# Kernel optimization log

Measured on AMD Instinct MI355X. Metric: run time of the kernel, lower is better.

The kernel has to match this reference:

```python
import jax, jax.numpy as jnp
import numpy as np

EMB = 1024
HEADS = 16
HD = EMB // HEADS

def setup_inputs() -> dict:
    key = jax.random.key(0)
    ks = jax.random.split(key, 9)
    s = 1.0 / np.sqrt(EMB)
    x = jax.random.normal(ks[0], (4, 2048, EMB), dtype=jnp.float32)
    Wq = jax.random.uniform(ks[1], (EMB, EMB), jnp.float32, -s, s)
    bq = jax.random.uniform(ks[2], (EMB,), jnp.float32, -s, s)
    Wk = jax.random.uniform(ks[3], (EMB, EMB), jnp.float32, -s, s)
    bk = jax.random.uniform(ks[4], (EMB,), jnp.float32, -s, s)
    Wv = jax.random.uniform(ks[5], (EMB, EMB), jnp.float32, -s, s)
    bv = jax.random.uniform(ks[6], (EMB,), jnp.float32, -s, s)
    Wo = jax.random.uniform(ks[7], (EMB, EMB), jnp.float32, -s, s)
    bo = jax.random.uniform(ks[8], (EMB,), jnp.float32, -s, s)
    return {"x": x, "Wq": Wq, "bq": bq, "Wk": Wk, "bk": bk, "Wv": Wv, "bv": bv, "Wo": Wo, "bo": bo}

def reference(x, Wq, bq, Wk, bk, Wv, bv, Wo, bo):
    B, T, C = x.shape
    # projections (torch Linear: y = x @ W^T + b)
    q = (x @ Wq.T + bq).reshape(B, T, HEADS, HD).transpose(0, 2, 1, 3)  # [B,H,T,hd]
    k = (x @ Wk.T + bk).reshape(B, T, HEADS, HD).transpose(0, 2, 1, 3)
    v = (x @ Wv.T + bv).reshape(B, T, HEADS, HD).transpose(0, 2, 1, 3)
    scores = jnp.einsum('bhqd,bhkd->bhqk', q, k) / jnp.sqrt(jnp.float32(HD))
    weights = jax.nn.softmax(scores, axis=-1)
    attn = jnp.einsum('bhqk,bhkd->bhqd', weights, v)
    out = attn.transpose(0, 2, 1, 3).reshape(B, T, C)
    return out @ Wo.T + bo
```

## Files before the change

kernel.cpp:

```cpp
#include <hip/hip_runtime.h>

#define TSEQ  2048
#define BATCH 4
#define NHEAD 16
#define EMB   1024

typedef __attribute__((ext_vector_type(8))) __bf16 bf16x8;
typedef __attribute__((ext_vector_type(4))) __bf16 bf16x4;
typedef __attribute__((ext_vector_type(4))) float  floatx4;
typedef __attribute__((ext_vector_type(2))) unsigned int uint32x2;
typedef __attribute__((ext_vector_type(4))) unsigned int uint32x4;

__device__ __forceinline__ void gload_lds16(const __bf16* g, __bf16* lds_uniform_base) {
  __builtin_amdgcn_global_load_lds(
      (__attribute__((address_space(1))) void*)(g),
      (__attribute__((address_space(3))) void*)(lds_uniform_base),
      16, 0, 0);
}

__global__ __launch_bounds__(256) void cvt_f32_bf16(
    const float* __restrict__ src, __bf16* __restrict__ dst)
{
  const int gid = (blockIdx.x * 256 + threadIdx.x) * 4;
  const float4 v = *(const float4*)(src + gid);
  dst[gid + 0] = (__bf16)v.x;
  dst[gid + 1] = (__bf16)v.y;
  dst[gid + 2] = (__bf16)v.z;
  dst[gid + 3] = (__bf16)v.w;
}

__global__ __launch_bounds__(256) void cvt_w4(
    const float* __restrict__ s0, const float* __restrict__ s1,
    const float* __restrict__ s2, const float* __restrict__ s3,
    __bf16* __restrict__ d0, __bf16* __restrict__ d1,
    __bf16* __restrict__ d2, __bf16* __restrict__ d3)
{
  const int z = blockIdx.z;
  const float* src = (z == 0) ? s0 : (z == 1) ? s1 : (z == 2) ? s2 : s3;
  __bf16*      dst = (z == 0) ? d0 : (z == 1) ? d1 : (z == 2) ? d2 : d3;
  const int gid = (blockIdx.x * 256 + threadIdx.x) * 4;
  const float4 v = *(const float4*)(src + gid);
  dst[gid + 0] = (__bf16)v.x;
  dst[gid + 1] = (__bf16)v.y;
  dst[gid + 2] = (__bf16)v.z;
  dst[gid + 3] = (__bf16)v.w;
}

__global__ __launch_bounds__(256) void gemm_bt_bias(
    const __bf16* __restrict__ A,
    const __bf16* __restrict__ W0, const __bf16* __restrict__ W1, const __bf16* __restrict__ W2,
    const float* __restrict__ B0, const float* __restrict__ B1, const float* __restrict__ B2,
    __bf16* __restrict__ C0, __bf16* __restrict__ C1, __bf16* __restrict__ C2)
{
  const int z = blockIdx.z;
  const __bf16* W  = (z == 0) ? W0 : ((z == 1) ? W1 : W2);
  const float*  Bb = (z == 0) ? B0 : ((z == 1) ? B1 : B2);
  __bf16*       C  = (z == 0) ? C0 : ((z == 1) ? C1 : C2);
  const float  scl = (z == 0) ? 0.125f * 1.44269504088896340736f : 1.0f;

  const int tid  = threadIdx.x;
  const int lane = tid & 63;
  const int wid  = tid >> 6;
  const int l16  = lane & 15;
  const int quad = lane >> 4;
  const int wm   = wid & 1;
  const int wn   = wid >> 1;
  const int lin = blockIdx.x + blockIdx.y * 8;
  const int swz = (lin & 7) * 64 + (lin >> 3);
  const int m0  = (swz >> 3) * 128;
  const int n0  = (swz & 7) * 128;

  __shared__ alignas(16) __bf16 As[128 * 32];
  __shared__ alignas(16) __bf16 Bs[128 * 32];

  floatx4 acc[4][4];
#pragma unroll
  for (int i = 0; i < 4; i++)
#pragma unroll
    for (int j = 0; j < 4; j++) acc[i][j] = (floatx4){0.f, 0.f, 0.f, 0.f};

  const int srow = tid >> 2;
  const int sseg = tid & 3;

  for (int k0 = 0; k0 < 1024; k0 += 32) {
    __syncthreads();
#pragma unroll
    for (int is = 0; is < 2; is++) {
      const int row = is * 64 + srow;
      gload_lds16(A + (size_t)(m0 + row) * 1024 + k0 + sseg * 8,
                  &As[(is * 256 + wid * 64) * 8]);
      gload_lds16(W + (size_t)(n0 + row) * 1024 + k0 + sseg * 8,
                  &Bs[(is * 256 + wid * 64) * 8]);
    }
    __syncthreads();

    bf16x8 af[4], bfr[4];
#pragma unroll
    for (int i = 0; i < 4; i++) {
      af[i]  = *(const bf16x8*)(&As[(wm * 64 + i * 16 + l16) * 32 + quad * 8]);
      bfr[i] = *(const bf16x8*)(&Bs[(wn * 64 + i * 16 + l16) * 32 + quad * 8]);
    }
#pragma unroll
    for (int i = 0; i < 4; i++)
#pragma unroll
      for (int j = 0; j < 4; j++)
        acc[i][j] = __builtin_amdgcn_mfma_f32_16x16x32_bf16(af[i], bfr[j], acc[i][j], 0, 0, 0);
  }

  float bv[4];
#pragma unroll
  for (int j = 0; j < 4; j++) bv[j] = Bb[n0 + wn * 64 + j * 16 + l16];

#pragma unroll
  for (int i = 0; i < 4; i++) {
    const size_t mrow = (size_t)m0 + wm * 64 + i * 16 + quad * 4;
#pragma unroll
    for (int j = 0; j < 4; j++) {
      const int col = n0 + wn * 64 + j * 16 + l16;
#pragma unroll
      for (int r = 0; r < 4; r++)
        C[(mrow + r) * 1024 + col] = (__bf16)((acc[i][j][r] + bv[j]) * scl);
    }
  }
}

__global__ __launch_bounds__(256) void gemm_bt_bias_f32(
    const __bf16* __restrict__ A, const __bf16* __restrict__ W,
    const float* __restrict__ Bb, float* __restrict__ C)
{
  const int tid  = threadIdx.x;
  const int lane = tid & 63;
  const int wid  = tid >> 6;
  const int l16  = lane & 15;
  const int quad = lane >> 4;
  const int wm   = wid & 1;
  const int wn   = wid >> 1;
  const int lin = blockIdx.x + blockIdx.y * 8;
  const int swz = (lin & 7) * 64 + (lin >> 3);
  const int m0  = (swz >> 3) * 128;
  const int n0  = (swz & 7) * 128;

  __shared__ alignas(16) __bf16 As[128 * 32];
  __shared__ alignas(16) __bf16 Bs[128 * 32];

  floatx4 acc[4][4];
#pragma unroll
  for (int i = 0; i < 4; i++)
#pragma unroll
    for (int j = 0; j < 4; j++) acc[i][j] = (floatx4){0.f, 0.f, 0.f, 0.f};

  const int srow = tid >> 2;
  const int sseg = tid & 3;

  for (int k0 = 0; k0 < 1024; k0 += 32) {
    __syncthreads();
#pragma unroll
    for (int is = 0; is < 2; is++) {
      const int row = is * 64 + srow;
      gload_lds16(A + (size_t)(m0 + row) * 1024 + k0 + sseg * 8,
                  &As[(is * 256 + wid * 64) * 8]);
      gload_lds16(W + (size_t)(n0 + row) * 1024 + k0 + sseg * 8,
                  &Bs[(is * 256 + wid * 64) * 8]);
    }
    __syncthreads();

    bf16x8 af[4], bfr[4];
#pragma unroll
    for (int i = 0; i < 4; i++) {
      af[i]  = *(const bf16x8*)(&As[(wm * 64 + i * 16 + l16) * 32 + quad * 8]);
      bfr[i] = *(const bf16x8*)(&Bs[(wn * 64 + i * 16 + l16) * 32 + quad * 8]);
    }
#pragma unroll
    for (int i = 0; i < 4; i++)
#pragma unroll
      for (int j = 0; j < 4; j++)
        acc[i][j] = __builtin_amdgcn_mfma_f32_16x16x32_bf16(af[i], bfr[j], acc[i][j], 0, 0, 0);
  }

  float bv[4];
#pragma unroll
  for (int j = 0; j < 4; j++) bv[j] = Bb[n0 + wn * 64 + j * 16 + l16];

#pragma unroll
  for (int i = 0; i < 4; i++) {
    const size_t mrow = (size_t)m0 + wm * 64 + i * 16 + quad * 4;
#pragma unroll
    for (int j = 0; j < 4; j++) {
      const int col = n0 + wn * 64 + j * 16 + l16;
#pragma unroll
      for (int r = 0; r < 4; r++)
        C[(mrow + r) * 1024 + col] = acc[i][j][r] + bv[j];
    }
  }
}

__global__ __launch_bounds__(256) void v_transpose(
    const __bf16* __restrict__ V, __bf16* __restrict__ VT)
{
  const int t0 = blockIdx.x * 64;
  const int bh = blockIdx.y;
  const int b  = bh >> 4;
  const int h  = bh & 15;
  const int tid = threadIdx.x;

  __shared__ alignas(16) __bf16 Ls[64 * 72];

  const int row = tid >> 2, seg = tid & 3;
  const __bf16* src = V + ((size_t)(b * TSEQ + t0 + row)) * EMB + h * 64;
  *(bf16x8*)(&Ls[row * 72 + seg * 8])       = *(const bf16x8*)(src + seg * 8);
  *(bf16x8*)(&Ls[row * 72 + (seg + 4) * 8]) = *(const bf16x8*)(src + (seg + 4) * 8);
  __syncthreads();

  const int od = tid >> 2, oseg = tid & 3;
  bf16x8 o0, o1;
#pragma unroll
  for (int j = 0; j < 8; j++) o0[j] = Ls[(oseg * 16 + j) * 72 + od];
#pragma unroll
  for (int j = 0; j < 8; j++) o1[j] = Ls[(oseg * 16 + 8 + j) * 72 + od];
  __bf16* dst = VT + ((size_t)bh * 64 + od) * TSEQ + t0 + oseg * 16;
  *(bf16x8*)(dst)     = o0;
  *(bf16x8*)(dst + 8) = o1;
}

#define KVB 64
#define NT  (TSEQ / KVB)

#define FA_ZERO (floatx4){0.f, 0.f, 0.f, 0.f}

#define FA_STAGE(BUF, TILE)                                                               \
  if ((TILE) < NT) {                                                                      \
    _Pragma("unroll")                                                                     \
    for (int c = 0; c < 2; c++) {                                                         \
      gload_lds16(kstage + (size_t)((TILE) * KVB + c * 8) * EMB,                          \
                  &Ks[BUF][(wid * 16 + c * 8) * 64]);                                     \
      gload_lds16(vstage + (size_t)(c * 8) * TSEQ + (TILE) * KVB,                         \
                  &VTs[BUF][(wid * 16 + c * 8) * 64]);                                    \
    }                                                                                     \
  }

#define SM_PACK(TA, TB, DST)                                                              \
  {                                                                                       \
    bf16x4 pa_, pb_;                                                                      \
    _Pragma("unroll")                                                                     \
    for (int r = 0; r < 4; r++) pa_[r] = (__bf16)__builtin_amdgcn_exp2f((TA)[r]);         \
    _Pragma("unroll")                                                                     \
    for (int r = 0; r < 4; r++) pb_[r] = (__bf16)__builtin_amdgcn_exp2f((TB)[r]);         \
    const uint32x2 A2_ = __builtin_bit_cast(uint32x2, pa_);                               \
    const uint32x2 B2_ = __builtin_bit_cast(uint32x2, pb_);                               \
    const uint32x2 r0_ = __builtin_amdgcn_permlane32_swap(A2_.x, B2_.x, false, false);    \
    const uint32x2 r1_ = __builtin_amdgcn_permlane32_swap(A2_.y, B2_.y, false, false);    \
    const uint32x2 s0_ = __builtin_amdgcn_permlane16_swap(r0_.x, r0_.y, false, false);    \
    const uint32x2 s1_ = __builtin_amdgcn_permlane16_swap(r1_.x, r1_.y, false, false);    \
    const uint32x4 fw_ = (uint32x4){s0_.x, s1_.x, s0_.y, s1_.y};                          \
    DST = __builtin_bit_cast(bf16x8, fw_);                                                \
  }

#define QK_BLOCK(BUF, KS, TA, TB)                                                         \
  {                                                                                       \
    const bf16x8 ka0 = *(const bf16x8*)(&Ks[BUF][(KS) * 2048 + aoff0]);                   \
    const bf16x8 ka1 = *(const bf16x8*)(&Ks[BUF][(KS) * 2048 + aoff1]);                   \
    const bf16x8 kb0 = *(const bf16x8*)(&Ks[BUF][(KS) * 2048 + 1024 + aoff0]);            \
    const bf16x8 kb1 = *(const bf16x8*)(&Ks[BUF][(KS) * 2048 + 1024 + aoff1]);            \
    _Pragma("unroll")                                                                     \
    for (int g = 0; g < 4; g++) {                                                         \
      TA[g] = FA_ZERO;                                                                    \
      TA[g] = __builtin_amdgcn_mfma_f32_16x16x32_bf16(ka0, qf[g][0], TA[g], 0, 0, 0);     \
      TA[g] = __builtin_amdgcn_mfma_f32_16x16x32_bf16(ka1, qf[g][1], TA[g], 0, 0, 0);     \
      TB[g] = FA_ZERO;                                                                    \
      TB[g] = __builtin_amdgcn_mfma_f32_16x16x32_bf16(kb0, qf[g][0], TB[g], 0, 0, 0);     \
      TB[g] = __builtin_amdgcn_mfma_f32_16x16x32_bf16(kb1, qf[g][1], TB[g], 0, 0, 0);     \
    }                                                                                     \
  }

#define FA_STEP(BUF, KT)                                                                  \
  {                                                                                       \
    __builtin_amdgcn_s_setprio(1);                                                        \
    bf16x8 vf[4][2];                                                                      \
    _Pragma("unroll")                                                                     \
    for (int dg = 0; dg < 4; dg++) {                                                      \
      vf[dg][0] = *(const bf16x8*)(&VTs[(BUF) ^ 1][dg * 1024 + aoff0]);                   \
      vf[dg][1] = *(const bf16x8*)(&VTs[(BUF) ^ 1][dg * 1024 + aoff1]);                   \
    }                                                                                     \
    floatx4 ta[4], tb[4];                                                                 \
    QK_BLOCK(BUF, 0, ta, tb)                                                              \
    _Pragma("unroll")                                                                     \
    for (int g = 0; g < 4; g++) {                                                         \
      bf16x8 nf;                                                                          \
      SM_PACK(ta[g], tb[g], nf)                                                           \
      _Pragma("unroll")                                                                   \
      for (int dg = 0; dg < 4; dg++)                                                      \
        Oacc[g][dg] = __builtin_amdgcn_mfma_f32_16x16x32_bf16(vf[dg][0], pfragP[g][0], Oacc[g][dg], 0, 0, 0); \
      lacc[g] = __builtin_amdgcn_mfma_f32_16x16x32_bf16(ones, pfragP[g][0], lacc[g], 0, 0, 0); \
      _Pragma("unroll")                                                                   \
      for (int dg = 0; dg < 4; dg++)                                                      \
        Oacc[g][dg] = __builtin_amdgcn_mfma_f32_16x16x32_bf16(vf[dg][1], pfragP[g][1], Oacc[g][dg], 0, 0, 0); \
      lacc[g] = __builtin_amdgcn_mfma_f32_16x16x32_bf16(ones, pfragP[g][1], lacc[g], 0, 0, 0); \
      pfragP[g][0] = nf;                                                                  \
    }                                                                                     \
    QK_BLOCK(BUF, 1, ta, tb)                                                              \
    __builtin_amdgcn_s_setprio(0);                                                        \
    __syncthreads();                                                                      \
    FA_STAGE((BUF) ^ 1, (KT) + 1);                                                        \
    _Pragma("unroll")                                                                     \
    for (int g = 0; g < 4; g++) { SM_PACK(ta[g], tb[g], pfragP[g][1]) }                   \
    __syncthreads();                                                                      \
  }

__global__ __launch_bounds__(256, 2) void flash_attn(
    const __bf16* __restrict__ Q, const __bf16* __restrict__ K,
    const __bf16* __restrict__ VT, __bf16* __restrict__ O)
{
  const int lin = blockIdx.x + blockIdx.y * 8;
  const int swz = (lin & 7) * 64 + (lin >> 3);
  const int qt  = swz & 7;
  const int bh  = swz >> 3;
  const int b    = bh >> 4;
  const int h    = bh & 15;
  const int tid  = threadIdx.x;
  const int wid  = tid >> 6;
  const int lane = tid & 63;
  const int l16  = lane & 15;
  const int quad = lane >> 4;

  __shared__ alignas(16) __bf16 Ks[2][KVB * 64];
  __shared__ alignas(16) __bf16 VTs[2][64 * 64];

  const size_t base = ((size_t)b * TSEQ) * EMB + (size_t)h * 64;
  const __bf16* qptr  = Q + base;
  const __bf16* kptr  = K + base;
  const __bf16* vtptr = VT + (size_t)bh * 64 * TSEQ;
  __bf16*       optr  = O + base;

  const int qb = qt * 256 + wid * 64;

  bf16x8 qf[4][2];
#pragma unroll
  for (int g = 0; g < 4; g++)
#pragma unroll
    for (int hf = 0; hf < 2; hf++)
      qf[g][hf] = *(const bf16x8*)(qptr + (size_t)(qb + g * 16 + l16) * EMB + hf * 32 + quad * 8);

  floatx4 Oacc[4][4];
#pragma unroll
  for (int g = 0; g < 4; g++)
#pragma unroll
    for (int dg = 0; dg < 4; dg++) Oacc[g][dg] = FA_ZERO;
  floatx4 lacc[4];
#pragma unroll
  for (int g = 0; g < 4; g++) lacc[g] = FA_ZERO;

  const uint32x4 onesw = (uint32x4){0x3F803F80u, 0x3F803F80u, 0x3F803F80u, 0x3F803F80u};
  const bf16x8 ones = __builtin_bit_cast(bf16x8, onesw);

  const int lrow = lane >> 3;
  const int xsg  = (lane & 7) ^ lrow;
  const __bf16* kstage = kptr  + (size_t)(wid * 16 + lrow) * EMB  + xsg * 8;
  const __bf16* vstage = vtptr + (size_t)(wid * 16 + lrow) * TSEQ + xsg * 8;

  const int h7    = l16 & 7;
  const int x0    = quad ^ h7;
  const int aoff0 = l16 * 64 + x0 * 8;
  const int aoff1 = l16 * 64 + (x0 ^ 4) * 8;

  bf16x8 pfragP[4][2];

  FA_STAGE(0, 0);
  __syncthreads();
  FA_STAGE(1, 1);
  {
    floatx4 ta[4], tb[4];
    QK_BLOCK(0, 0, ta, tb)
#pragma unroll
    for (int g = 0; g < 4; g++) { SM_PACK(ta[g], tb[g], pfragP[g][0]) }
    QK_BLOCK(0, 1, ta, tb)
#pragma unroll
    for (int g = 0; g < 4; g++) { SM_PACK(ta[g], tb[g], pfragP[g][1]) }
  }
  __syncthreads();

#pragma unroll 1
  for (int kt = 1; kt < NT - 1; kt += 2) {
    FA_STEP(1, kt);
    FA_STEP(0, kt + 1);
  }
  FA_STEP(1, NT - 1);

#pragma unroll
  for (int g = 0; g < 4; g++) {
#pragma unroll
    for (int dg = 0; dg < 4; dg++) {
      const bf16x8 v0 = *(const bf16x8*)(&VTs[1][dg * 1024 + aoff0]);
      const bf16x8 v1 = *(const bf16x8*)(&VTs[1][dg * 1024 + aoff1]);
      Oacc[g][dg] = __builtin_amdgcn_mfma_f32_16x16x32_bf16(v0, pfragP[g][0], Oacc[g][dg], 0, 0, 0);
      Oacc[g][dg] = __builtin_amdgcn_mfma_f32_16x16x32_bf16(v1, pfragP[g][1], Oacc[g][dg], 0, 0, 0);
    }
    lacc[g] = __builtin_amdgcn_mfma_f32_16x16x32_bf16(ones, pfragP[g][0], lacc[g], 0, 0, 0);
    lacc[g] = __builtin_amdgcn_mfma_f32_16x16x32_bf16(ones, pfragP[g][1], lacc[g], 0, 0, 0);
  }

#pragma unroll
  for (int g = 0; g < 4; g++) {
    const float inv = 1.0f / lacc[g][0];
#pragma unroll
    for (int dg = 0; dg < 4; dg++) {
      bf16x4 ov;
#pragma unroll
      for (int r = 0; r < 4; r++) ov[r] = (__bf16)(Oacc[g][dg][r] * inv);
      *(bf16x4*)(optr + (size_t)(qb + g * 16 + l16) * EMB + dg * 16 + quad * 4) = ov;
    }
  }
}

extern "C" void kernel_launch(void* const* d_in, const int* in_sizes, int n_in,
                              void* d_out, int out_size, void* d_ws, size_t ws_size,
                              hipStream_t stream) {
  const float* x  = (const float*)d_in[0];
  const float* Wq = (const float*)d_in[1];
  const float* bq = (const float*)d_in[2];
  const float* Wk = (const float*)d_in[3];
  const float* bk = (const float*)d_in[4];
  const float* Wv = (const float*)d_in[5];
  const float* bv = (const float*)d_in[6];
  const float* Wo = (const float*)d_in[7];
  const float* bo = (const float*)d_in[8];
  float* out = (float*)d_out;

  const size_t NELEM = (size_t)BATCH * TSEQ * EMB;
  const size_t WELEM = (size_t)EMB * EMB;

  __bf16* q_b  = (__bf16*)d_out;
  __bf16* k_b  = q_b + NELEM;
  __bf16* x_b  = (__bf16*)d_ws;
  __bf16* v_b  = x_b + NELEM;
  __bf16* wq_b = v_b + NELEM;
  __bf16* wk_b = wq_b + WELEM;
  __bf16* wv_b = wk_b + WELEM;
  __bf16* wo_b = wv_b + WELEM;

  dim3 blk(256, 1, 1);

  cvt_f32_bf16<<<(int)(NELEM / 1024), blk, 0, stream>>>(x, x_b);
  cvt_w4<<<dim3((int)(WELEM / 1024), 1, 4), blk, 0, stream>>>(
      Wq, Wk, Wv, Wo, wq_b, wk_b, wv_b, wo_b);

  gemm_bt_bias<<<dim3(8, 64, 3), blk, 0, stream>>>(
      x_b, wq_b, wk_b, wv_b, bq, bk, bv, q_b, k_b, v_b);

  v_transpose<<<dim3(TSEQ / 64, BATCH * NHEAD), blk, 0, stream>>>(v_b, x_b);

  flash_attn<<<dim3(TSEQ / 256, BATCH * NHEAD), blk, 0, stream>>>(
      q_b, k_b, x_b, v_b);

  gemm_bt_bias_f32<<<dim3(8, 64, 1), blk, 0, stream>>>(v_b, wo_b, bo, out);
}
```

Measured before the change: 261.1 us.

## Double-buffer GEMM with swizzled LDS and shrink flash-attention query tile

The QKV and output GEMMs now share a macro body that uses a 64-wide K tile, double-buffered LDS with XOR-swizzled rows, and explicit vmcnt waits, so global loads overlap MFMA work and LDS bank conflicts drop. Flash attention is cut from 256 to 128 query rows per block, 32 per wave, which doubles the grid and lowers register pressure. V fragments are also read from LDS inside the MFMA loop instead of being preloaded. The trade-offs are more LDS per GEMM block, twice the K/V tile reloads in attention, and correctness that depends on the hand-written waitcnt and barrier sequence.

```diff
diff --git a/kernel.cpp b/kernel.cpp
--- a/kernel.cpp
+++ b/kernel.cpp
@@ -46,6 +46,89 @@
   dst[gid + 3] = (__bf16)v.w;
 }
 
+#define GK_NT 16
+
+#define GEMM_STAGE(BUF, K0)                                                               \
+  {                                                                                       \
+    _Pragma("unroll")                                                                     \
+    for (int c = 0; c < 4; c++) {                                                         \
+      gload_lds16(aStage + (size_t)(c * 32) * 1024 + (K0),                                \
+                  &As[BUF][(c * 32 + wid * 8) * 64]);                                     \
+      gload_lds16(bStage + (size_t)(c * 32) * 1024 + (K0),                                \
+                  &Bs[BUF][(c * 32 + wid * 8) * 64]);                                     \
+    }                                                                                     \
+  }
+
+#define GEMM_BODY(C_STORE)                                                                \
+  const int tid  = threadIdx.x;                                                           \
+  const int lane = tid & 63;                                                              \
+  const int wid  = tid >> 6;                                                              \
+  const int l16  = lane & 15;                                                             \
+  const int quad = lane >> 4;                                                             \
+  const int wm   = wid & 1;                                                               \
+  const int wn   = wid >> 1;                                                              \
+  const int lin = blockIdx.x + blockIdx.y * 8;                                            \
+  const int swz = (lin & 7) * 64 + (lin >> 3);                                            \
+  const int m0  = (swz >> 3) * 128;                                                       \
+  const int n0  = (swz & 7) * 128;                                                        \
+  __shared__ alignas(16) __bf16 As[2][128 * 64];                                          \
+  __shared__ alignas(16) __bf16 Bs[2][128 * 64];                                          \
+  floatx4 acc[4][4];                                                                      \
+  _Pragma("unroll")                                                                       \
+  for (int i = 0; i < 4; i++)                                                             \
+    _Pragma("unroll")                                                                     \
+    for (int j = 0; j < 4; j++) acc[i][j] = (floatx4){0.f, 0.f, 0.f, 0.f};                \
+  const int lrow = lane >> 3;                                                             \
+  const int xsg  = (lane & 7) ^ lrow;                                                     \
+  const __bf16* aStage = A + (size_t)(m0 + wid * 8 + lrow) * 1024 + xsg * 8;              \
+  const __bf16* bStage = W + (size_t)(n0 + wid * 8 + lrow) * 1024 + xsg * 8;              \
+  const int h7 = l16 & 7;                                                                 \
+  GEMM_STAGE(0, 0)                                                                        \
+  GEMM_STAGE(1, 64)                                                                       \
+  __asm__ __volatile__("s_waitcnt vmcnt(8)\n\ts_barrier" ::: "memory");                   \
+  int cur = 0;                                                                            \
+  _Pragma("unroll 1")                                                                     \
+  for (int k = 0; k < GK_NT; ++k) {                                                       \
+    bf16x8 af0[4], af1[4], bf0[4], bf1[4];                                                \
+    _Pragma("unroll")                                                                     \
+    for (int i = 0; i < 4; i++) {                                                         \
+      const int ar = (wm * 64 + i * 16 + l16) * 64;                                       \
+      const int br = (wn * 64 + i * 16 + l16) * 64;                                       \
+      af0[i] = *(const bf16x8*)(&As[cur][ar + ((quad ^ h7)) * 8]);                        \
+      af1[i] = *(const bf16x8*)(&As[cur][ar + (((4 + quad) ^ h7)) * 8]);                  \
+      bf0[i] = *(const bf16x8*)(&Bs[cur][br + ((quad ^ h7)) * 8]);                        \
+      bf1[i] = *(const bf16x8*)(&Bs[cur][br + (((4 + quad) ^ h7)) * 8]);                  \
+    }                                                                                     \
+    _Pragma("unroll")                                                                     \
+    for (int i = 0; i < 4; i++)                                                           \
+      _Pragma("unroll")                                                                   \
+      for (int j = 0; j < 4; j++) {                                                       \
+        acc[i][j] = __builtin_amdgcn_mfma_f32_16x16x32_bf16(af0[i], bf0[j], acc[i][j], 0, 0, 0); \
+        acc[i][j] = __builtin_amdgcn_mfma_f32_16x16x32_bf16(af1[i], bf1[j], acc[i][j], 0, 0, 0); \
+      }                                                                                   \
+    __asm__ __volatile__("s_waitcnt lgkmcnt(0)\n\ts_barrier" ::: "memory");               \
+    if (k < GK_NT - 2) {                                                                  \
+      GEMM_STAGE(cur, (k + 2) * 64)                                                       \
+      __asm__ __volatile__("s_waitcnt vmcnt(8)\n\ts_barrier" ::: "memory");               \
+    } else if (k == GK_NT - 2) {                                                          \
+      __asm__ __volatile__("s_waitcnt vmcnt(0)\n\ts_barrier" ::: "memory");               \
+    }                                                                                     \
+    cur ^= 1;                                                                             \
+  }                                                                                       \
+  float bv[4];                                                                            \
+  _Pragma("unroll")                                                                       \
+  for (int j = 0; j < 4; j++) bv[j] = Bb[n0 + wn * 64 + j * 16 + l16];                    \
+  _Pragma("unroll")                                                                       \
+  for (int i = 0; i < 4; i++) {                                                           \
+    const size_t mrow = (size_t)m0 + wm * 64 + i * 16 + quad * 4;                         \
+    _Pragma("unroll")                                                                     \
+    for (int j = 0; j < 4; j++) {                                                         \
+      const int col = n0 + wn * 64 + j * 16 + l16;                                        \
+      _Pragma("unroll")                                                                   \
+      for (int r = 0; r < 4; r++) C_STORE;                                                \
+    }                                                                                     \
+  }
+
 __global__ __launch_bounds__(256) void gemm_bt_bias(
     const __bf16* __restrict__ A,
     const __bf16* __restrict__ W0, const __bf16* __restrict__ W1, const __bf16* __restrict__ W2,
@@ -57,141 +140,14 @@
   const float*  Bb = (z == 0) ? B0 : ((z == 1) ? B1 : B2);
   __bf16*       C  = (z == 0) ? C0 : ((z == 1) ? C1 : C2);
   const float  scl = (z == 0) ? 0.125f * 1.44269504088896340736f : 1.0f;
-
-  const int tid  = threadIdx.x;
-  const int lane = tid & 63;
-  const int wid  = tid >> 6;
-  const int l16  = lane & 15;
-  const int quad = lane >> 4;
-  const int wm   = wid & 1;
-  const int wn   = wid >> 1;
-  const int lin = blockIdx.x + blockIdx.y * 8;
-  const int swz = (lin & 7) * 64 + (lin >> 3);
-  const int m0  = (swz >> 3) * 128;
-  const int n0  = (swz & 7) * 128;
-
-  __shared__ alignas(16) __bf16 As[128 * 32];
-  __shared__ alignas(16) __bf16 Bs[128 * 32];
-
-  floatx4 acc[4][4];
-#pragma unroll
-  for (int i = 0; i < 4; i++)
-#pragma unroll
-    for (int j = 0; j < 4; j++) acc[i][j] = (floatx4){0.f, 0.f, 0.f, 0.f};
-
-  const int srow = tid >> 2;
-  const int sseg = tid & 3;
-
-  for (int k0 = 0; k0 < 1024; k0 += 32) {
-    __syncthreads();
-#pragma unroll
-    for (int is = 0; is < 2; is++) {
-      const int row = is * 64 + srow;
-      gload_lds16(A + (size_t)(m0 + row) * 1024 + k0 + sseg * 8,
-                  &As[(is * 256 + wid * 64) * 8]);
-      gload_lds16(W + (size_t)(n0 + row) * 1024 + k0 + sseg * 8,
-                  &Bs[(is * 256 + wid * 64) * 8]);
-    }
-    __syncthreads();
-
-    bf16x8 af[4], bfr[4];
-#pragma unroll
-    for (int i = 0; i < 4; i++) {
-      af[i]  = *(const bf16x8*)(&As[(wm * 64 + i * 16 + l16) * 32 + quad * 8]);
-      bfr[i] = *(const bf16x8*)(&Bs[(wn * 64 + i * 16 + l16) * 32 + quad * 8]);
-    }
-#pragma unroll
-    for (int i = 0; i < 4; i++)
-#pragma unroll
-      for (int j = 0; j < 4; j++)
-        acc[i][j] = __builtin_amdgcn_mfma_f32_16x16x32_bf16(af[i], bfr[j], acc[i][j], 0, 0, 0);
-  }
-
-  float bv[4];
-#pragma unroll
-  for (int j = 0; j < 4; j++) bv[j] = Bb[n0 + wn * 64 + j * 16 + l16];
-
-#pragma unroll
-  for (int i = 0; i < 4; i++) {
-    const size_t mrow = (size_t)m0 + wm * 64 + i * 16 + quad * 4;
-#pragma unroll
-    for (int j = 0; j < 4; j++) {
-      const int col = n0 + wn * 64 + j * 16 + l16;
-#pragma unroll
-      for (int r = 0; r < 4; r++)
-        C[(mrow + r) * 1024 + col] = (__bf16)((acc[i][j][r] + bv[j]) * scl);
-    }
-  }
+  GEMM_BODY(C[(mrow + r) * 1024 + col] = (__bf16)((acc[i][j][r] + bv[j]) * scl))
 }
 
 __global__ __launch_bounds__(256) void gemm_bt_bias_f32(
     const __bf16* __restrict__ A, const __bf16* __restrict__ W,
     const float* __restrict__ Bb, float* __restrict__ C)
 {
-  const int tid  = threadIdx.x;
-  const int lane = tid & 63;
-  const int wid  = tid >> 6;
-  const int l16  = lane & 15;
-  const int quad = lane >> 4;
-  const int wm   = wid & 1;
-  const int wn   = wid >> 1;
-  const int lin = blockIdx.x + blockIdx.y * 8;
-  const int swz = (lin & 7) * 64 + (lin >> 3);
-  const int m0  = (swz >> 3) * 128;
-  const int n0  = (swz & 7) * 128;
-
-  __shared__ alignas(16) __bf16 As[128 * 32];
-  __shared__ alignas(16) __bf16 Bs[128 * 32];
-
-  floatx4 acc[4][4];
-#pragma unroll
-  for (int i = 0; i < 4; i++)
-#pragma unroll
-    for (int j = 0; j < 4; j++) acc[i][j] = (floatx4){0.f, 0.f, 0.f, 0.f};
-
-  const int srow = tid >> 2;
-  const int sseg = tid & 3;
-
-  for (int k0 = 0; k0 < 1024; k0 += 32) {
-    __syncthreads();
-#pragma unroll
-    for (int is = 0; is < 2; is++) {
-      const int row = is * 64 + srow;
-      gload_lds16(A + (size_t)(m0 + row) * 1024 + k0 + sseg * 8,
-                  &As[(is * 256 + wid * 64) * 8]);
-      gload_lds16(W + (size_t)(n0 + row) * 1024 + k0 + sseg * 8,
-                  &Bs[(is * 256 + wid * 64) * 8]);
-    }
-    __syncthreads();
-
-    bf16x8 af[4], bfr[4];
-#pragma unroll
-    for (int i = 0; i < 4; i++) {
-      af[i]  = *(const bf16x8*)(&As[(wm * 64 + i * 16 + l16) * 32 + quad * 8]);
-      bfr[i] = *(const bf16x8*)(&Bs[(wn * 64 + i * 16 + l16) * 32 + quad * 8]);
-    }
-#pragma unroll
-    for (int i = 0; i < 4; i++)
-#pragma unroll
-      for (int j = 0; j < 4; j++)
-        acc[i][j] = __builtin_amdgcn_mfma_f32_16x16x32_bf16(af[i], bfr[j], acc[i][j], 0, 0, 0);
-  }
-
-  float bv[4];
-#pragma unroll
-  for (int j = 0; j < 4; j++) bv[j] = Bb[n0 + wn * 64 + j * 16 + l16];
-
-#pragma unroll
-  for (int i = 0; i < 4; i++) {
-    const size_t mrow = (size_t)m0 + wm * 64 + i * 16 + quad * 4;
-#pragma unroll
-    for (int j = 0; j < 4; j++) {
-      const int col = n0 + wn * 64 + j * 16 + l16;
-#pragma unroll
-      for (int r = 0; r < 4; r++)
-        C[(mrow + r) * 1024 + col] = acc[i][j][r] + bv[j];
-    }
-  }
+  GEMM_BODY(C[(mrow + r) * 1024 + col] = acc[i][j][r] + bv[j])
 }
 
 __global__ __launch_bounds__(256) void v_transpose(
@@ -262,7 +218,7 @@
     const bf16x8 kb0 = *(const bf16x8*)(&Ks[BUF][(KS) * 2048 + 1024 + aoff0]);            \
     const bf16x8 kb1 = *(const bf16x8*)(&Ks[BUF][(KS) * 2048 + 1024 + aoff1]);            \
     _Pragma("unroll")                                                                     \
-    for (int g = 0; g < 4; g++) {                                                         \
+    for (int g = 0; g < 2; g++) {                                                         \
       TA[g] = FA_ZERO;                                                                    \
       TA[g] = __builtin_amdgcn_mfma_f32_16x16x32_bf16(ka0, qf[g][0], TA[g], 0, 0, 0);     \
       TA[g] = __builtin_amdgcn_mfma_f32_16x16x32_bf16(ka1, qf[g][1], TA[g], 0, 0, 0);     \
@@ -275,25 +231,23 @@
 #define FA_STEP(BUF, KT)                                                                  \
   {                                                                                       \
     __builtin_amdgcn_s_setprio(1);                                                        \
-    bf16x8 vf[4][2];                                                                      \
-    _Pragma("unroll")                                                                     \
-    for (int dg = 0; dg < 4; dg++) {                                                      \
-      vf[dg][0] = *(const bf16x8*)(&VTs[(BUF) ^ 1][dg * 1024 + aoff0]);                   \
-      vf[dg][1] = *(const bf16x8*)(&VTs[(BUF) ^ 1][dg * 1024 + aoff1]);                   \
-    }                                                                                     \
-    floatx4 ta[4], tb[4];                                                                 \
+    floatx4 ta[2], tb[2];                                                                 \
     QK_BLOCK(BUF, 0, ta, tb)                                                              \
     _Pragma("unroll")                                                                     \
-    for (int g = 0; g < 4; g++) {                                                         \
+    for (int g = 0; g < 2; g++) {                                                         \
       bf16x8 nf;                                                                          \
       SM_PACK(ta[g], tb[g], nf)                                                           \
       _Pragma("unroll")                                                                   \
-      for (int dg = 0; dg < 4; dg++)                                                      \
-        Oacc[g][dg] = __builtin_amdgcn_mfma_f32_16x16x32_bf16(vf[dg][0], pfragP[g][0], Oacc[g][dg], 0, 0, 0); \
+      for (int dg = 0; dg < 4; dg++) {                                                    \
+        const bf16x8 v0 = *(const bf16x8*)(&VTs[(BUF) ^ 1][dg * 1024 + aoff0]);           \
+        Oacc[g][dg] = __builtin_amdgcn_mfma_f32_16x16x32_bf16(v0, pfragP[g][0], Oacc[g][dg], 0, 0, 0); \
+      }                                                                                   \
       lacc[g] = __builtin_amdgcn_mfma_f32_16x16x32_bf16(ones, pfragP[g][0], lacc[g], 0, 0, 0); \
       _Pragma("unroll")                                                                   \
-      for (int dg = 0; dg < 4; dg++)                                                      \
-        Oacc[g][dg] = __builtin_amdgcn_mfma_f32_16x16x32_bf16(vf[dg][1], pfragP[g][1], Oacc[g][dg], 0, 0, 0); \
+      for (int dg = 0; dg < 4; dg++) {                                                    \
+        const bf16x8 v1 = *(const bf16x8*)(&VTs[(BUF) ^ 1][dg * 1024 + aoff1]);           \
+        Oacc[g][dg] = __builtin_amdgcn_mfma_f32_16x16x32_bf16(v1, pfragP[g][1], Oacc[g][dg], 0, 0, 0); \
+      }                                                                                   \
       lacc[g] = __builtin_amdgcn_mfma_f32_16x16x32_bf16(ones, pfragP[g][1], lacc[g], 0, 0, 0); \
       pfragP[g][0] = nf;                                                                  \
     }                                                                                     \
@@ -302,7 +256,7 @@
     __syncthreads();                                                                      \
     FA_STAGE((BUF) ^ 1, (KT) + 1);                                                        \
     _Pragma("unroll")                                                                     \
-    for (int g = 0; g < 4; g++) { SM_PACK(ta[g], tb[g], pfragP[g][1]) }                   \
+    for (int g = 0; g < 2; g++) { SM_PACK(ta[g], tb[g], pfragP[g][1]) }                   \
     __syncthreads();                                                                      \
   }
 
@@ -310,10 +264,10 @@
     const __bf16* __restrict__ Q, const __bf16* __restrict__ K,
     const __bf16* __restrict__ VT, __bf16* __restrict__ O)
 {
-  const int lin = blockIdx.x + blockIdx.y * 8;
-  const int swz = (lin & 7) * 64 + (lin >> 3);
-  const int qt  = swz & 7;
-  const int bh  = swz >> 3;
+  const int lin = blockIdx.x + blockIdx.y * 16;
+  const int swz = (lin & 7) * 128 + (lin >> 3);
+  const int qt  = swz & 15;
+  const int bh  = swz >> 4;
   const int b    = bh >> 4;
   const int h    = bh & 15;
   const int tid  = threadIdx.x;
@@ -331,23 +285,23 @@
   const __bf16* vtptr = VT + (size_t)bh * 64 * TSEQ;
   __bf16*       optr  = O + base;
 
-  const int qb = qt * 256 + wid * 64;
-
-  bf16x8 qf[4][2];
-#pragma unroll
-  for (int g = 0; g < 4; g++)
+  const int qb = qt * 128 + wid * 32;
+
+  bf16x8 qf[2][2];
+#pragma unroll
+  for (int g = 0; g < 2; g++)
 #pragma unroll
     for (int hf = 0; hf < 2; hf++)
       qf[g][hf] = *(const bf16x8*)(qptr + (size_t)(qb + g * 16 + l16) * EMB + hf * 32 + quad * 8);
 
-  floatx4 Oacc[4][4];
-#pragma unroll
-  for (int g = 0; g < 4; g++)
+  floatx4 Oacc[2][4];
+#pragma unroll
+  for (int g = 0; g < 2; g++)
 #pragma unroll
     for (int dg = 0; dg < 4; dg++) Oacc[g][dg] = FA_ZERO;
-  floatx4 lacc[4];
-#pragma unroll
-  for (int g = 0; g < 4; g++) lacc[g] = FA_ZERO;
+  floatx4 lacc[2];
+#pragma unroll
+  for (int g = 0; g < 2; g++) lacc[g] = FA_ZERO;
 
   const uint32x4 onesw = (uint32x4){0x3F803F80u, 0x3F803F80u, 0x3F803F80u, 0x3F803F80u};
   const bf16x8 ones = __builtin_bit_cast(bf16x8, onesw);
@@ -362,19 +316,19 @@
   const int aoff0 = l16 * 64 + x0 * 8;
   const int aoff1 = l16 * 64 + (x0 ^ 4) * 8;
 
-  bf16x8 pfragP[4][2];
+  bf16x8 pfragP[2][2];
 
   FA_STAGE(0, 0);
   __syncthreads();
   FA_STAGE(1, 1);
   {
-    floatx4 ta[4], tb[4];
+    floatx4 ta[2], tb[2];
     QK_BLOCK(0, 0, ta, tb)
 #pragma unroll
-    for (int g = 0; g < 4; g++) { SM_PACK(ta[g], tb[g], pfragP[g][0]) }
+    for (int g = 0; g < 2; g++) { SM_PACK(ta[g], tb[g], pfragP[g][0]) }
     QK_BLOCK(0, 1, ta, tb)
 #pragma unroll
-    for (int g = 0; g < 4; g++) { SM_PACK(ta[g], tb[g], pfragP[g][1]) }
+    for (int g = 0; g < 2; g++) { SM_PACK(ta[g], tb[g], pfragP[g][1]) }
   }
   __syncthreads();
 
@@ -386,7 +340,7 @@
   FA_STEP(1, NT - 1);
 
 #pragma unroll
-  for (int g = 0; g < 4; g++) {
+  for (int g = 0; g < 2; g++) {
 #pragma unroll
     for (int dg = 0; dg < 4; dg++) {
       const bf16x8 v0 = *(const bf16x8*)(&VTs[1][dg * 1024 + aoff0]);
@@ -399,7 +353,7 @@
   }
 
 #pragma unroll
-  for (int g = 0; g < 4; g++) {
+  for (int g = 0; g < 2; g++) {
     const float inv = 1.0f / lacc[g][0];
 #pragma unroll
     for (int dg = 0; dg < 4; dg++) {
@@ -448,7 +402,7 @@
 
   v_transpose<<<dim3(TSEQ / 64, BATCH * NHEAD), blk, 0, stream>>>(v_b, x_b);
 
-  flash_attn<<<dim3(TSEQ / 256, BATCH * NHEAD), blk, 0, stream>>>(
+  flash_attn<<<dim3(TSEQ / 128, BATCH * NHEAD), blk, 0, stream>>>(
       q_b, k_b, x_b, v_b);
 
   gemm_bt_bias_f32<<<dim3(8, 64, 1), blk, 0, stream>>>(v_b, wo_b, bo, out);
```

After: 265.9 us. About the same (+1.9%).
